# Performance work log

Measured on AMD Instinct MI355X. Metric: run time of the kernel, lower is better.

Reference implementation:

```python
import jax, jax.numpy as jnp
import numpy as np

D_K = 128


def setup_inputs() -> dict:
    key = jax.random.key(0)
    kq, kk, kv = jax.random.split(key, 3)
    S = 8192
    Query = jax.random.normal(kq, (S, D_K), dtype=jnp.float32)
    Key = jax.random.normal(kk, (S, D_K), dtype=jnp.float32)
    Value = jax.random.normal(kv, (S, D_K), dtype=jnp.float32)
    return {"Query": Query, "Key": Key, "Value": Value}


def reference(Query, Key, Value):
    # scaled dot-product attention, unmasked (masked=False default)
    scale = 1.0 / jnp.sqrt(jnp.asarray(D_K, dtype=jnp.float32))
    scores = jnp.matmul(Query, Key.T) * scale          # [S, S]
    attn = jax.nn.softmax(scores, axis=1)              # softmax over keys (dim=1 on 2-D)
    delta_E = jnp.matmul(attn, Value)                  # [S, d_k]
    return delta_E
```

## Files before the change

kernel.cpp:

```cpp
#include <hip/hip_runtime.h>

#define S_LEN 8192
#define D_KK  128
#define SCALE 0.08838834764831845f

typedef __bf16 bf16x2 __attribute__((ext_vector_type(2)));
typedef __bf16 bf16x4 __attribute__((ext_vector_type(4)));
typedef __bf16 bf16x8 __attribute__((ext_vector_type(8)));
typedef float  f32x16 __attribute__((ext_vector_type(16)));
typedef _Float16 half_t;

__global__ __launch_bounds__(256) void prep_kv_23450521436217(
    const float* __restrict__ K,
    const float* __restrict__ V,
    __bf16* __restrict__ Kf,
    __bf16* __restrict__ Vf)
{
    const int tid = threadIdx.x;
    const int t   = blockIdx.x;
    __shared__ __bf16 T[32][140];

    const float* ktile = K + (size_t)t * 32 * D_KK;
    const float* vtile = V + (size_t)t * 32 * D_KK;

    const int row = tid & 31;
    const int cp  = tid >> 5;
    #pragma unroll
    for (int i = 0; i < 2; ++i) {
        int c = cp * 2 + i;
        int s = c >> 1, hi = c & 1;
        const float* src = ktile + row * D_KK + c * 8;
        float4 a = *(const float4*)(src);
        float4 b = *(const float4*)(src + 4);
        bf16x8 o;
        o[0]=(__bf16)a.x; o[1]=(__bf16)a.y; o[2]=(__bf16)a.z; o[3]=(__bf16)a.w;
        o[4]=(__bf16)b.x; o[5]=(__bf16)b.y; o[6]=(__bf16)b.z; o[7]=(__bf16)b.w;
        *(bf16x8*)(Kf + (size_t)(t * 8 + s) * 512 + hi * 256 + row * 8) = o;
    }

    #pragma unroll
    for (int i = 0; i < 4; ++i) {
        int f4 = tid + i * 256;
        float4 v = ((const float4*)vtile)[f4];
        int r = f4 >> 5, cc = (f4 & 31) << 2;
        bf16x4 b;
        b[0]=(__bf16)v.x; b[1]=(__bf16)v.y; b[2]=(__bf16)v.z; b[3]=(__bf16)v.w;
        *(bf16x4*)(&T[r][cc]) = b;
    }
    __syncthreads();

    #pragma unroll
    for (int i = 0; i < 2; ++i) {
        int idx  = tid + i * 256;
        int frag = idx >> 6, lane = idx & 63;
        int hi = lane >> 5, l5 = lane & 31;
        int d = frag >> 1, h = frag & 1;
        bf16x8 o;
        #pragma unroll
        for (int j = 0; j < 8; ++j) o[j] = T[16 * h + 8 * hi + j][32 * d + l5];
        *(bf16x8*)(Vf + (size_t)(t * 8 + frag) * 512 + lane * 8) = o;
    }
}

__global__ __launch_bounds__(512, 2) void attn_part_23450521436217(
    const float*  __restrict__ Q,
    const __bf16* __restrict__ Kf,
    const __bf16* __restrict__ Vf,
    half_t* __restrict__ P16,
    float*  __restrict__ Mp,
    float*  __restrict__ Lp)
{
    const int tid  = threadIdx.x;
    const int wave = tid >> 6;
    const int lane = tid & 63;
    const int l5   = lane & 31;
    const int hi   = lane >> 5;

    const int ks   = blockIdx.x & 7;
    const int qt   = blockIdx.x >> 3;
    const int qsub = qt * 8 + wave;
    const int qrow = qsub * 32 + l5;

    __shared__ __align__(16) __bf16 Klds[2][4096];

    bf16x8 qf[8];
    #pragma unroll
    for (int s = 0; s < 8; ++s) {
        const float* qp = Q + (size_t)qrow * D_KK + s * 16 + hi * 8;
        float4 a = *(const float4*)(qp);
        float4 b = *(const float4*)(qp + 4);
        bf16x8 f;
        f[0]=(__bf16)(a.x*SCALE); f[1]=(__bf16)(a.y*SCALE);
        f[2]=(__bf16)(a.z*SCALE); f[3]=(__bf16)(a.w*SCALE);
        f[4]=(__bf16)(b.x*SCALE); f[5]=(__bf16)(b.y*SCALE);
        f[6]=(__bf16)(b.z*SCALE); f[7]=(__bf16)(b.w*SCALE);
        qf[s] = f;
    }

    f32x16 oacc[4];
    #pragma unroll
    for (int d = 0; d < 4; ++d) oacc[d] = f32x16{};
    float m_run = -1e30f, l_run = 0.0f;

    const __bf16* kbase = Kf + (size_t)(ks * 32) * 4096;
    const __bf16* vfp   = Vf + (size_t)(ks * 32) * 4096 + lane * 8;

    {
        const __bf16* src = kbase + wave * 512 + lane * 8;
        __builtin_amdgcn_global_load_lds(
            (const __attribute__((address_space(1))) void*)src,
            (__attribute__((address_space(3))) void*)&Klds[0][wave * 512],
            16, 0, 0);
    }
    __syncthreads();

    for (int it = 0; it < 32; ++it) {
        const int cur = it & 1;

        if (it < 31) {
            const __bf16* src = kbase + (size_t)(it + 1) * 4096 + wave * 512 + lane * 8;
            __builtin_amdgcn_global_load_lds(
                (const __attribute__((address_space(1))) void*)src,
                (__attribute__((address_space(3))) void*)&Klds[cur ^ 1][wave * 512],
                16, 0, 0);
        }

        const __bf16* vt = vfp + (size_t)it * 4096;
        bf16x8 vb[8];
        #pragma unroll
        for (int f = 0; f < 8; ++f) vb[f] = *(const bf16x8*)(vt + f * 512);

        f32x16 c = f32x16{};
        __builtin_amdgcn_s_setprio(1);
        #pragma unroll
        for (int s = 0; s < 8; ++s) {
            bf16x8 kf = *(const bf16x8*)(&Klds[cur][s * 512 + lane * 8]);
            c = __builtin_amdgcn_mfma_f32_32x32x16_bf16(kf, qf[s], c, 0, 0, 0);
        }
        __builtin_amdgcn_s_setprio(0);

        float x0 = fmaxf(c[0], c[8]),  x1 = fmaxf(c[1], c[9]);
        float x2 = fmaxf(c[2], c[10]), x3 = fmaxf(c[3], c[11]);
        float x4 = fmaxf(c[4], c[12]), x5 = fmaxf(c[5], c[13]);
        float x6 = fmaxf(c[6], c[14]), x7 = fmaxf(c[7], c[15]);
        float y0 = fmaxf(fmaxf(x0, x4), fmaxf(x1, x5));
        float y1 = fmaxf(fmaxf(x2, x6), fmaxf(x3, x7));
        float tmax = fmaxf(y0, y1);
        tmax = fmaxf(tmax, __shfl_xor(tmax, 32));
        if (__any(tmax > m_run + 8.0f)) {
            float mnew  = fmaxf(m_run, tmax);
            float alpha = __expf(m_run - mnew);
            #pragma unroll
            for (int d = 0; d < 4; ++d) oacc[d] *= alpha;
            l_run *= alpha;
            m_run  = mnew;
        }
        float p[16];
        #pragma unroll
        for (int r = 0; r < 16; ++r) p[r] = __expf(c[r] - m_run);
        float s0a = (p[0]+p[1]) + (p[2]+p[3]),   s1a = (p[4]+p[5]) + (p[6]+p[7]);
        float s2a = (p[8]+p[9]) + (p[10]+p[11]), s3a = (p[12]+p[13]) + (p[14]+p[15]);
        float ps = (s0a + s1a) + (s2a + s3a);
        ps += __shfl_xor(ps, 32);
        l_run += ps;

        unsigned pk[8];
        #pragma unroll
        for (int tq = 0; tq < 8; ++tq) {
            bf16x2 w; w[0] = (__bf16)p[2*tq]; w[1] = (__bf16)p[2*tq+1];
            pk[tq] = __builtin_bit_cast(unsigned, w);
        }
        asm volatile("v_permlane32_swap_b32 %0, %1" : "+v"(pk[0]), "+v"(pk[2]));
        asm volatile("v_permlane32_swap_b32 %0, %1" : "+v"(pk[1]), "+v"(pk[3]));
        asm volatile("v_permlane32_swap_b32 %0, %1" : "+v"(pk[4]), "+v"(pk[6]));
        asm volatile("v_permlane32_swap_b32 %0, %1" : "+v"(pk[5]), "+v"(pk[7]));
        union { unsigned u[4]; bf16x8 f; } b0, b1;
        b0.u[0]=pk[0]; b0.u[1]=pk[1]; b0.u[2]=pk[2]; b0.u[3]=pk[3];
        b1.u[0]=pk[4]; b1.u[1]=pk[5]; b1.u[2]=pk[6]; b1.u[3]=pk[7];

        __builtin_amdgcn_s_setprio(1);
        #pragma unroll
        for (int d = 0; d < 4; ++d) {
            oacc[d] = __builtin_amdgcn_mfma_f32_32x32x16_bf16(vb[2*d+0], b0.f,
                                                              oacc[d], 0,0,0);
            oacc[d] = __builtin_amdgcn_mfma_f32_32x32x16_bf16(vb[2*d+1], b1.f,
                                                              oacc[d], 0,0,0);
        }
        __builtin_amdgcn_s_setprio(0);

        __syncthreads();
    }

    if (lane < 32) {
        Mp[ks * S_LEN + qrow] = m_run;
        Lp[ks * S_LEN + qrow] = l_run;
    }
    half_t* pb = P16 + (size_t)(ks * 256 + qsub) * (128 * 32);
    #pragma unroll
    for (int d = 0; d < 4; ++d)
        #pragma unroll
        for (int reg = 0; reg < 16; ++reg) {
            int drow = d * 32 + (reg & 3) + 8 * (reg >> 2) + 4 * hi;
            pb[drow * 32 + l5] = (half_t)oacc[d][reg];
        }
}

__global__ __launch_bounds__(256) void attn_merge_23450521436217(
    const half_t* __restrict__ P16,
    const float*  __restrict__ Mp,
    const float*  __restrict__ Lp,
    float* __restrict__ O)
{
    const int tid  = threadIdx.x;
    const int qsub = blockIdx.x;

    __shared__ float W[8][32];
    __shared__ float Li[32];
    __shared__ float Ot[128][33];

    if (tid < 32) {
        const int qrow = qsub * 32 + tid;
        float m[8], l[8];
        #pragma unroll
        for (int ks = 0; ks < 8; ++ks) {
            m[ks] = Mp[ks * S_LEN + qrow];
            l[ks] = Lp[ks * S_LEN + qrow];
        }
        float M = m[0];
        #pragma unroll
        for (int ks = 1; ks < 8; ++ks) M = fmaxf(M, m[ks]);
        float L = 0.0f;
        #pragma unroll
        for (int ks = 0; ks < 8; ++ks) {
            float w = __expf(m[ks] - M);
            W[ks][tid] = w;
            L += l[ks] * w;
        }
        Li[tid] = 1.0f / L;
    }
    __syncthreads();

    const int q  = tid & 31;
    const int dg = tid >> 5;
    #pragma unroll
    for (int j = 0; j < 16; ++j) {
        const int d = dg * 16 + j;
        float acc = 0.0f;
        #pragma unroll
        for (int ks = 0; ks < 8; ++ks)
            acc += W[ks][q] *
                   (float)P16[(size_t)(ks * 256 + qsub) * (128 * 32) + d * 32 + q];
        Ot[d][q] = acc;
    }
    __syncthreads();

    const int qq = tid >> 3;
    const int dv = (tid & 7) * 16;
    const float il = Li[qq];
    float* op = O + (size_t)(qsub * 32 + qq) * D_KK + dv;
    #pragma unroll
    for (int i = 0; i < 4; ++i) {
        float4 o;
        o.x = Ot[dv + i*4 + 0][qq] * il;
        o.y = Ot[dv + i*4 + 1][qq] * il;
        o.z = Ot[dv + i*4 + 2][qq] * il;
        o.w = Ot[dv + i*4 + 3][qq] * il;
        ((float4*)op)[i] = o;
    }
}

extern "C" void kernel_launch(void* const* d_in, const int* in_sizes, int n_in,
                              void* d_out, int out_size, void* d_ws, size_t ws_size,
                              hipStream_t stream) {
    const float* Q = (const float*)d_in[0];
    const float* K = (const float*)d_in[1];
    const float* V = (const float*)d_in[2];
    float* O = (float*)d_out;

    char* ws = (char*)d_ws;
    const size_t kf_b = (size_t)S_LEN * D_KK * 2;
    __bf16* Kf = (__bf16*)(ws);
    __bf16* Vf = (__bf16*)(ws + kf_b);
    float*  Mp = (float*) (ws + 2 * kf_b);
    float*  Lp = (float*) (ws + 2 * kf_b + 8 * S_LEN * 4);
    half_t* P16= (half_t*)(ws + 2 * kf_b + 16 * S_LEN * 4);

    hipLaunchKernelGGL(prep_kv_23450521436217, dim3(S_LEN/32), dim3(256), 0, stream,
                       K, V, Kf, Vf);
    hipLaunchKernelGGL(attn_part_23450521436217, dim3(256), dim3(512), 0, stream,
                       Q, Kf, Vf, P16, Mp, Lp);
    hipLaunchKernelGGL(attn_merge_23450521436217, dim3(S_LEN/32), dim3(256), 0, stream,
                       P16, Mp, Lp, O);
}
```

Measured before the change: 63.83 us.

## Split each block's KV range across two wave groups and fold log2e into Q scale

After: 228.7 us. 258% more time.

```diff
diff --git a/kernel.cpp b/kernel.cpp
--- a/kernel.cpp
+++ b/kernel.cpp
@@ -2,7 +2,7 @@
 
 #define S_LEN 8192
 #define D_KK  128
-#define SCALE 0.08838834764831845f
+#define SCALE2 (0.08838834764831845f * 1.44269504088896340f)
 
 typedef __bf16 bf16x2 __attribute__((ext_vector_type(2)));
 typedef __bf16 bf16x4 __attribute__((ext_vector_type(4)));
@@ -62,7 +62,7 @@
     }
 }
 
-__global__ __launch_bounds__(512, 2) void attn_part_23450521436217(
+__global__ __launch_bounds__(1024, 4) void attn_part_23450521436217(
     const float*  __restrict__ Q,
     const __bf16* __restrict__ Kf,
     const __bf16* __restrict__ Vf,
@@ -75,13 +75,16 @@
     const int lane = tid & 63;
     const int l5   = lane & 31;
     const int hi   = lane >> 5;
+    const int wq   = wave & 7;
+    const int kvh  = wave >> 3;
 
     const int ks   = blockIdx.x & 7;
     const int qt   = blockIdx.x >> 3;
-    const int qsub = qt * 8 + wave;
+    const int qsub = qt * 8 + wq;
     const int qrow = qsub * 32 + l5;
 
-    __shared__ __align__(16) __bf16 Klds[2][4096];
+    __shared__ __align__(16) __bf16 Klds[2][2][4096];
+    __shared__ float Mx[8][32], Lx[8][32];
 
     bf16x8 qf[8];
     #pragma unroll
@@ -90,10 +93,10 @@
         float4 a = *(const float4*)(qp);
         float4 b = *(const float4*)(qp + 4);
         bf16x8 f;
-        f[0]=(__bf16)(a.x*SCALE); f[1]=(__bf16)(a.y*SCALE);
-        f[2]=(__bf16)(a.z*SCALE); f[3]=(__bf16)(a.w*SCALE);
-        f[4]=(__bf16)(b.x*SCALE); f[5]=(__bf16)(b.y*SCALE);
-        f[6]=(__bf16)(b.z*SCALE); f[7]=(__bf16)(b.w*SCALE);
+        f[0]=(__bf16)(a.x*SCALE2); f[1]=(__bf16)(a.y*SCALE2);
+        f[2]=(__bf16)(a.z*SCALE2); f[3]=(__bf16)(a.w*SCALE2);
+        f[4]=(__bf16)(b.x*SCALE2); f[5]=(__bf16)(b.y*SCALE2);
+        f[6]=(__bf16)(b.z*SCALE2); f[7]=(__bf16)(b.w*SCALE2);
         qf[s] = f;
     }
 
@@ -102,26 +105,26 @@
     for (int d = 0; d < 4; ++d) oacc[d] = f32x16{};
     float m_run = -1e30f, l_run = 0.0f;
 
-    const __bf16* kbase = Kf + (size_t)(ks * 32) * 4096;
-    const __bf16* vfp   = Vf + (size_t)(ks * 32) * 4096 + lane * 8;
+    const __bf16* kbase = Kf + (size_t)(ks * 32 + kvh * 16) * 4096;
+    const __bf16* vfp   = Vf + (size_t)(ks * 32 + kvh * 16) * 4096 + lane * 8;
 
     {
-        const __bf16* src = kbase + wave * 512 + lane * 8;
+        const __bf16* src = kbase + wq * 512 + lane * 8;
         __builtin_amdgcn_global_load_lds(
             (const __attribute__((address_space(1))) void*)src,
-            (__attribute__((address_space(3))) void*)&Klds[0][wave * 512],
+            (__attribute__((address_space(3))) void*)&Klds[kvh][0][wq * 512],
             16, 0, 0);
     }
     __syncthreads();
 
-    for (int it = 0; it < 32; ++it) {
+    for (int it = 0; it < 16; ++it) {
         const int cur = it & 1;
 
-        if (it < 31) {
-            const __bf16* src = kbase + (size_t)(it + 1) * 4096 + wave * 512 + lane * 8;
+        if (it < 15) {
+            const __bf16* src = kbase + (size_t)(it + 1) * 4096 + wq * 512 + lane * 8;
             __builtin_amdgcn_global_load_lds(
                 (const __attribute__((address_space(1))) void*)src,
-                (__attribute__((address_space(3))) void*)&Klds[cur ^ 1][wave * 512],
+                (__attribute__((address_space(3))) void*)&Klds[kvh][cur ^ 1][wq * 512],
                 16, 0, 0);
         }
 
@@ -134,7 +137,7 @@
         __builtin_amdgcn_s_setprio(1);
         #pragma unroll
         for (int s = 0; s < 8; ++s) {
-            bf16x8 kf = *(const bf16x8*)(&Klds[cur][s * 512 + lane * 8]);
+            bf16x8 kf = *(const bf16x8*)(&Klds[kvh][cur][s * 512 + lane * 8]);
             c = __builtin_amdgcn_mfma_f32_32x32x16_bf16(kf, qf[s], c, 0, 0, 0);
         }
         __builtin_amdgcn_s_setprio(0);
@@ -147,9 +150,9 @@
         float y1 = fmaxf(fmaxf(x2, x6), fmaxf(x3, x7));
         float tmax = fmaxf(y0, y1);
         tmax = fmaxf(tmax, __shfl_xor(tmax, 32));
-        if (__any(tmax > m_run + 8.0f)) {
+        if (__any(tmax > m_run + 11.5f)) {
             float mnew  = fmaxf(m_run, tmax);
-            float alpha = __expf(m_run - mnew);
+            float alpha = exp2f(m_run - mnew);
             #pragma unroll
             for (int d = 0; d < 4; ++d) oacc[d] *= alpha;
             l_run *= alpha;
@@ -157,7 +160,7 @@
         }
         float p[16];
         #pragma unroll
-        for (int r = 0; r < 16; ++r) p[r] = __expf(c[r] - m_run);
+        for (int r = 0; r < 16; ++r) p[r] = exp2f(c[r] - m_run);
         float s0a = (p[0]+p[1]) + (p[2]+p[3]),   s1a = (p[4]+p[5]) + (p[6]+p[7]);
         float s2a = (p[8]+p[9]) + (p[10]+p[11]), s3a = (p[12]+p[13]) + (p[14]+p[15]);
         float ps = (s0a + s1a) + (s2a + s3a);
@@ -191,18 +194,43 @@
         __syncthreads();
     }
 
-    if (lane < 32) {
-        Mp[ks * S_LEN + qrow] = m_run;
-        Lp[ks * S_LEN + qrow] = l_run;
-    }
-    half_t* pb = P16 + (size_t)(ks * 256 + qsub) * (128 * 32);
-    #pragma unroll
-    for (int d = 0; d < 4; ++d)
-        #pragma unroll
-        for (int reg = 0; reg < 16; ++reg) {
-            int drow = d * 32 + (reg & 3) + 8 * (reg >> 2) + 4 * hi;
-            pb[drow * 32 + l5] = (half_t)oacc[d][reg];
-        }
+    half_t* mrgbase = (half_t*)Klds;
+
+    if (kvh == 1 && lane < 32) { Mx[wq][lane] = m_run; Lx[wq][lane] = l_run; }
+
+    for (int r = 0; r < 2; ++r) {
+        if (kvh == 1 && (wq >> 2) == r) {
+            half_t* mb = mrgbase + (size_t)(wq & 3) * 4096;
+            #pragma unroll
+            for (int d = 0; d < 4; ++d)
+                #pragma unroll
+                for (int reg = 0; reg < 16; ++reg) {
+                    int drow = d * 32 + (reg & 3) + 8 * (reg >> 2) + 4 * hi;
+                    mb[drow * 32 + l5] = (half_t)oacc[d][reg];
+                }
+        }
+        __syncthreads();
+        if (kvh == 0 && (wq >> 2) == r) {
+            float m1 = Mx[wq][l5], l1 = Lx[wq][l5];
+            float M  = fmaxf(m_run, m1);
+            float w0 = exp2f(m_run - M), w1 = exp2f(m1 - M);
+            if (lane < 32) {
+                Mp[ks * S_LEN + qrow] = M;
+                Lp[ks * S_LEN + qrow] = l_run * w0 + l1 * w1;
+            }
+            const half_t* mb = mrgbase + (size_t)(wq & 3) * 4096;
+            half_t* pb = P16 + (size_t)(ks * 256 + qsub) * 4096;
+            #pragma unroll
+            for (int d = 0; d < 4; ++d)
+                #pragma unroll
+                for (int reg = 0; reg < 16; ++reg) {
+                    int drow = d * 32 + (reg & 3) + 8 * (reg >> 2) + 4 * hi;
+                    pb[drow * 32 + l5] =
+                        (half_t)(oacc[d][reg] * w0 + (float)mb[drow * 32 + l5] * w1);
+                }
+        }
+        __syncthreads();
+    }
 }
 
 __global__ __launch_bounds__(256) void attn_merge_23450521436217(
@@ -232,7 +260,7 @@
         float L = 0.0f;
         #pragma unroll
         for (int ks = 0; ks < 8; ++ks) {
-            float w = __expf(m[ks] - M);
+            float w = exp2f(m[ks] - M);
             W[ks][tid] = w;
             L += l[ks] * w;
         }
@@ -287,7 +315,7 @@
 
     hipLaunchKernelGGL(prep_kv_23450521436217, dim3(S_LEN/32), dim3(256), 0, stream,
                        K, V, Kf, Vf);
-    hipLaunchKernelGGL(attn_part_23450521436217, dim3(256), dim3(512), 0, stream,
+    hipLaunchKernelGGL(attn_part_23450521436217, dim3(256), dim3(1024), 0, stream,
                        Q, Kf, Vf, P16, Mp, Lp);
     hipLaunchKernelGGL(attn_merge_23450521436217, dim3(S_LEN/32), dim3(256), 0, stream,
                        P16, Mp, Lp, O);
```

## Split output head dimension across two wave groups and use exp2 softmax

Applied to the files above, without the earlier changes.

Result: slower. 90.56 us (+41.9%).

```diff
diff --git a/kernel.cpp b/kernel.cpp
--- a/kernel.cpp
+++ b/kernel.cpp
@@ -2,7 +2,7 @@
 
 #define S_LEN 8192
 #define D_KK  128
-#define SCALE 0.08838834764831845f
+#define SCALE2 (0.08838834764831845f * 1.44269504088896340f)
 
 typedef __bf16 bf16x2 __attribute__((ext_vector_type(2)));
 typedef __bf16 bf16x4 __attribute__((ext_vector_type(4)));
@@ -62,7 +62,7 @@
     }
 }
 
-__global__ __launch_bounds__(512, 2) void attn_part_23450521436217(
+__global__ __launch_bounds__(1024, 1) void attn_part_23450521436217(
     const float*  __restrict__ Q,
     const __bf16* __restrict__ Kf,
     const __bf16* __restrict__ Vf,
@@ -75,10 +75,12 @@
     const int lane = tid & 63;
     const int l5   = lane & 31;
     const int hi   = lane >> 5;
+    const int wq   = wave & 7;
+    const int dh   = wave >> 3;
 
     const int ks   = blockIdx.x & 7;
     const int qt   = blockIdx.x >> 3;
-    const int qsub = qt * 8 + wave;
+    const int qsub = qt * 8 + wq;
     const int qrow = qsub * 32 + l5;
 
     __shared__ __align__(16) __bf16 Klds[2][4096];
@@ -90,26 +92,25 @@
         float4 a = *(const float4*)(qp);
         float4 b = *(const float4*)(qp + 4);
         bf16x8 f;
-        f[0]=(__bf16)(a.x*SCALE); f[1]=(__bf16)(a.y*SCALE);
-        f[2]=(__bf16)(a.z*SCALE); f[3]=(__bf16)(a.w*SCALE);
-        f[4]=(__bf16)(b.x*SCALE); f[5]=(__bf16)(b.y*SCALE);
-        f[6]=(__bf16)(b.z*SCALE); f[7]=(__bf16)(b.w*SCALE);
+        f[0]=(__bf16)(a.x*SCALE2); f[1]=(__bf16)(a.y*SCALE2);
+        f[2]=(__bf16)(a.z*SCALE2); f[3]=(__bf16)(a.w*SCALE2);
+        f[4]=(__bf16)(b.x*SCALE2); f[5]=(__bf16)(b.y*SCALE2);
+        f[6]=(__bf16)(b.z*SCALE2); f[7]=(__bf16)(b.w*SCALE2);
         qf[s] = f;
     }
 
-    f32x16 oacc[4];
-    #pragma unroll
-    for (int d = 0; d < 4; ++d) oacc[d] = f32x16{};
+    f32x16 oacc0 = f32x16{}, oacc1 = f32x16{};
     float m_run = -1e30f, l_run = 0.0f;
 
     const __bf16* kbase = Kf + (size_t)(ks * 32) * 4096;
-    const __bf16* vfp   = Vf + (size_t)(ks * 32) * 4096 + lane * 8;
-
-    {
-        const __bf16* src = kbase + wave * 512 + lane * 8;
+    const __bf16* vfp   = Vf + (size_t)(ks * 32) * 4096 + lane * 8
+                             + (size_t)(dh * 4) * 512;
+
+    if (dh == 0) {
+        const __bf16* src = kbase + wq * 512 + lane * 8;
         __builtin_amdgcn_global_load_lds(
             (const __attribute__((address_space(1))) void*)src,
-            (__attribute__((address_space(3))) void*)&Klds[0][wave * 512],
+            (__attribute__((address_space(3))) void*)&Klds[0][wq * 512],
             16, 0, 0);
     }
     __syncthreads();
@@ -117,18 +118,13 @@
     for (int it = 0; it < 32; ++it) {
         const int cur = it & 1;
 
-        if (it < 31) {
-            const __bf16* src = kbase + (size_t)(it + 1) * 4096 + wave * 512 + lane * 8;
+        if (dh == 0 && it < 31) {
+            const __bf16* src = kbase + (size_t)(it + 1) * 4096 + wq * 512 + lane * 8;
             __builtin_amdgcn_global_load_lds(
                 (const __attribute__((address_space(1))) void*)src,
-                (__attribute__((address_space(3))) void*)&Klds[cur ^ 1][wave * 512],
+                (__attribute__((address_space(3))) void*)&Klds[cur ^ 1][wq * 512],
                 16, 0, 0);
         }
-
-        const __bf16* vt = vfp + (size_t)it * 4096;
-        bf16x8 vb[8];
-        #pragma unroll
-        for (int f = 0; f < 8; ++f) vb[f] = *(const bf16x8*)(vt + f * 512);
 
         f32x16 c = f32x16{};
         __builtin_amdgcn_s_setprio(1);
@@ -147,17 +143,17 @@
         float y1 = fmaxf(fmaxf(x2, x6), fmaxf(x3, x7));
         float tmax = fmaxf(y0, y1);
         tmax = fmaxf(tmax, __shfl_xor(tmax, 32));
-        if (__any(tmax > m_run + 8.0f)) {
+        if (__any(tmax > m_run + 11.5f)) {
             float mnew  = fmaxf(m_run, tmax);
-            float alpha = __expf(m_run - mnew);
-            #pragma unroll
-            for (int d = 0; d < 4; ++d) oacc[d] *= alpha;
+            float alpha = exp2f(m_run - mnew);
+            oacc0 *= alpha;
+            oacc1 *= alpha;
             l_run *= alpha;
             m_run  = mnew;
         }
         float p[16];
         #pragma unroll
-        for (int r = 0; r < 16; ++r) p[r] = __expf(c[r] - m_run);
+        for (int r = 0; r < 16; ++r) p[r] = exp2f(c[r] - m_run);
         float s0a = (p[0]+p[1]) + (p[2]+p[3]),   s1a = (p[4]+p[5]) + (p[6]+p[7]);
         float s2a = (p[8]+p[9]) + (p[10]+p[11]), s3a = (p[12]+p[13]) + (p[14]+p[15]);
         float ps = (s0a + s1a) + (s2a + s3a);
@@ -178,31 +174,34 @@
         b0.u[0]=pk[0]; b0.u[1]=pk[1]; b0.u[2]=pk[2]; b0.u[3]=pk[3];
         b1.u[0]=pk[4]; b1.u[1]=pk[5]; b1.u[2]=pk[6]; b1.u[3]=pk[7];
 
+        const __bf16* vt = vfp + (size_t)it * 4096;
+        bf16x8 v0 = *(const bf16x8*)(vt);
+        bf16x8 v1 = *(const bf16x8*)(vt + 512);
+        bf16x8 v2 = *(const bf16x8*)(vt + 1024);
+        bf16x8 v3 = *(const bf16x8*)(vt + 1536);
+
         __builtin_amdgcn_s_setprio(1);
-        #pragma unroll
-        for (int d = 0; d < 4; ++d) {
-            oacc[d] = __builtin_amdgcn_mfma_f32_32x32x16_bf16(vb[2*d+0], b0.f,
-                                                              oacc[d], 0,0,0);
-            oacc[d] = __builtin_amdgcn_mfma_f32_32x32x16_bf16(vb[2*d+1], b1.f,
-                                                              oacc[d], 0,0,0);
-        }
+        oacc0 = __builtin_amdgcn_mfma_f32_32x32x16_bf16(v0, b0.f, oacc0, 0, 0, 0);
+        oacc0 = __builtin_amdgcn_mfma_f32_32x32x16_bf16(v1, b1.f, oacc0, 0, 0, 0);
+        oacc1 = __builtin_amdgcn_mfma_f32_32x32x16_bf16(v2, b0.f, oacc1, 0, 0, 0);
+        oacc1 = __builtin_amdgcn_mfma_f32_32x32x16_bf16(v3, b1.f, oacc1, 0, 0, 0);
         __builtin_amdgcn_s_setprio(0);
 
         __syncthreads();
     }
 
-    if (lane < 32) {
+    if (dh == 0 && lane < 32) {
         Mp[ks * S_LEN + qrow] = m_run;
         Lp[ks * S_LEN + qrow] = l_run;
     }
-    half_t* pb = P16 + (size_t)(ks * 256 + qsub) * (128 * 32);
-    #pragma unroll
-    for (int d = 0; d < 4; ++d)
-        #pragma unroll
-        for (int reg = 0; reg < 16; ++reg) {
-            int drow = d * 32 + (reg & 3) + 8 * (reg >> 2) + 4 * hi;
-            pb[drow * 32 + l5] = (half_t)oacc[d][reg];
-        }
+    half_t* pb = P16 + (size_t)(ks * 256 + qsub) * 4096;
+    #pragma unroll
+    for (int reg = 0; reg < 16; ++reg) {
+        int drow0 = (2*dh + 0) * 32 + (reg & 3) + 8 * (reg >> 2) + 4 * hi;
+        int drow1 = (2*dh + 1) * 32 + (reg & 3) + 8 * (reg >> 2) + 4 * hi;
+        pb[drow0 * 32 + l5] = (half_t)oacc0[reg];
+        pb[drow1 * 32 + l5] = (half_t)oacc1[reg];
+    }
 }
 
 __global__ __launch_bounds__(256) void attn_merge_23450521436217(
@@ -232,7 +231,7 @@
         float L = 0.0f;
         #pragma unroll
         for (int ks = 0; ks < 8; ++ks) {
-            float w = __expf(m[ks] - M);
+            float w = exp2f(m[ks] - M);
             W[ks][tid] = w;
             L += l[ks] * w;
         }
@@ -287,7 +286,7 @@
 
     hipLaunchKernelGGL(prep_kv_23450521436217, dim3(S_LEN/32), dim3(256), 0, stream,
                        K, V, Kf, Vf);
-    hipLaunchKernelGGL(attn_part_23450521436217, dim3(256), dim3(512), 0, stream,
+    hipLaunchKernelGGL(attn_part_23450521436217, dim3(256), dim3(1024), 0, stream,
                        Q, Kf, Vf, P16, Mp, Lp);
     hipLaunchKernelGGL(attn_merge_23450521436217, dim3(S_LEN/32), dim3(256), 0, stream,
                        P16, Mp, Lp, O);
```

## Use 16-way KV split and exp2-based softmax with folded log2e scale

Applied to the files above, without the earlier changes.

Result: slower. 111.9 us (+75.4%).

```diff
diff --git a/kernel.cpp b/kernel.cpp
--- a/kernel.cpp
+++ b/kernel.cpp
@@ -2,7 +2,7 @@
 
 #define S_LEN 8192
 #define D_KK  128
-#define SCALE 0.08838834764831845f
+#define SCALE2 (0.08838834764831845f * 1.44269504088896340f)
 
 typedef __bf16 bf16x2 __attribute__((ext_vector_type(2)));
 typedef __bf16 bf16x4 __attribute__((ext_vector_type(4)));
@@ -62,6 +62,7 @@
     }
 }
 
+template<int NS>
 __global__ __launch_bounds__(512, 2) void attn_part_23450521436217(
     const float*  __restrict__ Q,
     const __bf16* __restrict__ Kf,
@@ -70,14 +71,15 @@
     float*  __restrict__ Mp,
     float*  __restrict__ Lp)
 {
+    constexpr int ITERS = 256 / NS;
     const int tid  = threadIdx.x;
     const int wave = tid >> 6;
     const int lane = tid & 63;
     const int l5   = lane & 31;
     const int hi   = lane >> 5;
 
-    const int ks   = blockIdx.x & 7;
-    const int qt   = blockIdx.x >> 3;
+    const int ks   = blockIdx.x & (NS - 1);
+    const int qt   = blockIdx.x / NS;
     const int qsub = qt * 8 + wave;
     const int qrow = qsub * 32 + l5;
 
@@ -90,10 +92,10 @@
         float4 a = *(const float4*)(qp);
         float4 b = *(const float4*)(qp + 4);
         bf16x8 f;
-        f[0]=(__bf16)(a.x*SCALE); f[1]=(__bf16)(a.y*SCALE);
-        f[2]=(__bf16)(a.z*SCALE); f[3]=(__bf16)(a.w*SCALE);
-        f[4]=(__bf16)(b.x*SCALE); f[5]=(__bf16)(b.y*SCALE);
-        f[6]=(__bf16)(b.z*SCALE); f[7]=(__bf16)(b.w*SCALE);
+        f[0]=(__bf16)(a.x*SCALE2); f[1]=(__bf16)(a.y*SCALE2);
+        f[2]=(__bf16)(a.z*SCALE2); f[3]=(__bf16)(a.w*SCALE2);
+        f[4]=(__bf16)(b.x*SCALE2); f[5]=(__bf16)(b.y*SCALE2);
+        f[6]=(__bf16)(b.z*SCALE2); f[7]=(__bf16)(b.w*SCALE2);
         qf[s] = f;
     }
 
@@ -102,8 +104,8 @@
     for (int d = 0; d < 4; ++d) oacc[d] = f32x16{};
     float m_run = -1e30f, l_run = 0.0f;
 
-    const __bf16* kbase = Kf + (size_t)(ks * 32) * 4096;
-    const __bf16* vfp   = Vf + (size_t)(ks * 32) * 4096 + lane * 8;
+    const __bf16* kbase = Kf + (size_t)(ks * ITERS) * 4096;
+    const __bf16* vfp   = Vf + (size_t)(ks * ITERS) * 4096 + lane * 8;
 
     {
         const __bf16* src = kbase + wave * 512 + lane * 8;
@@ -114,10 +116,10 @@
     }
     __syncthreads();
 
-    for (int it = 0; it < 32; ++it) {
+    for (int it = 0; it < ITERS; ++it) {
         const int cur = it & 1;
 
-        if (it < 31) {
+        if (it < ITERS - 1) {
             const __bf16* src = kbase + (size_t)(it + 1) * 4096 + wave * 512 + lane * 8;
             __builtin_amdgcn_global_load_lds(
                 (const __attribute__((address_space(1))) void*)src,
@@ -147,9 +149,9 @@
         float y1 = fmaxf(fmaxf(x2, x6), fmaxf(x3, x7));
         float tmax = fmaxf(y0, y1);
         tmax = fmaxf(tmax, __shfl_xor(tmax, 32));
-        if (__any(tmax > m_run + 8.0f)) {
+        if (__any(tmax > m_run + 11.5f)) {
             float mnew  = fmaxf(m_run, tmax);
-            float alpha = __expf(m_run - mnew);
+            float alpha = exp2f(m_run - mnew);
             #pragma unroll
             for (int d = 0; d < 4; ++d) oacc[d] *= alpha;
             l_run *= alpha;
@@ -157,7 +159,7 @@
         }
         float p[16];
         #pragma unroll
-        for (int r = 0; r < 16; ++r) p[r] = __expf(c[r] - m_run);
+        for (int r = 0; r < 16; ++r) p[r] = exp2f(c[r] - m_run);
         float s0a = (p[0]+p[1]) + (p[2]+p[3]),   s1a = (p[4]+p[5]) + (p[6]+p[7]);
         float s2a = (p[8]+p[9]) + (p[10]+p[11]), s3a = (p[12]+p[13]) + (p[14]+p[15]);
         float ps = (s0a + s1a) + (s2a + s3a);
@@ -205,6 +207,7 @@
         }
 }
 
+template<int NS>
 __global__ __launch_bounds__(256) void attn_merge_23450521436217(
     const half_t* __restrict__ P16,
     const float*  __restrict__ Mp,
@@ -214,25 +217,25 @@
     const int tid  = threadIdx.x;
     const int qsub = blockIdx.x;
 
-    __shared__ float W[8][32];
+    __shared__ float W[NS][32];
     __shared__ float Li[32];
     __shared__ float Ot[128][33];
 
     if (tid < 32) {
         const int qrow = qsub * 32 + tid;
-        float m[8], l[8];
-        #pragma unroll
-        for (int ks = 0; ks < 8; ++ks) {
+        float m[NS], l[NS];
+        #pragma unroll
+        for (int ks = 0; ks < NS; ++ks) {
             m[ks] = Mp[ks * S_LEN + qrow];
             l[ks] = Lp[ks * S_LEN + qrow];
         }
         float M = m[0];
         #pragma unroll
-        for (int ks = 1; ks < 8; ++ks) M = fmaxf(M, m[ks]);
+        for (int ks = 1; ks < NS; ++ks) M = fmaxf(M, m[ks]);
         float L = 0.0f;
         #pragma unroll
-        for (int ks = 0; ks < 8; ++ks) {
-            float w = __expf(m[ks] - M);
+        for (int ks = 0; ks < NS; ++ks) {
+            float w = exp2f(m[ks] - M);
             W[ks][tid] = w;
             L += l[ks] * w;
         }
@@ -247,7 +250,7 @@
         const int d = dg * 16 + j;
         float acc = 0.0f;
         #pragma unroll
-        for (int ks = 0; ks < 8; ++ks)
+        for (int ks = 0; ks < NS; ++ks)
             acc += W[ks][q] *
                    (float)P16[(size_t)(ks * 256 + qsub) * (128 * 32) + d * 32 + q];
         Ot[d][q] = acc;
@@ -281,14 +284,27 @@
     const size_t kf_b = (size_t)S_LEN * D_KK * 2;
     __bf16* Kf = (__bf16*)(ws);
     __bf16* Vf = (__bf16*)(ws + kf_b);
-    float*  Mp = (float*) (ws + 2 * kf_b);
-    float*  Lp = (float*) (ws + 2 * kf_b + 8 * S_LEN * 4);
-    half_t* P16= (half_t*)(ws + 2 * kf_b + 16 * S_LEN * 4);
 
     hipLaunchKernelGGL(prep_kv_23450521436217, dim3(S_LEN/32), dim3(256), 0, stream,
                        K, V, Kf, Vf);
-    hipLaunchKernelGGL(attn_part_23450521436217, dim3(256), dim3(512), 0, stream,
-                       Q, Kf, Vf, P16, Mp, Lp);
-    hipLaunchKernelGGL(attn_merge_23450521436217, dim3(S_LEN/32), dim3(256), 0, stream,
-                       P16, Mp, Lp, O);
+
+    const size_t need16 = 2 * kf_b + (size_t)2 * 16 * S_LEN * 4
+                        + (size_t)16 * 256 * 4096 * 2;
+    if (ws_size >= need16) {
+        float*  Mp = (float*) (ws + 2 * kf_b);
+        float*  Lp = (float*) (ws + 2 * kf_b + 16 * S_LEN * 4);
+        half_t* P16= (half_t*)(ws + 2 * kf_b + 32 * S_LEN * 4);
+        hipLaunchKernelGGL((attn_part_23450521436217<16>), dim3(512), dim3(512),
+                           0, stream, Q, Kf, Vf, P16, Mp, Lp);
+        hipLaunchKernelGGL((attn_merge_23450521436217<16>), dim3(S_LEN/32), dim3(256),
+                           0, stream, P16, Mp, Lp, O);
+    } else {
+        float*  Mp = (float*) (ws + 2 * kf_b);
+        float*  Lp = (float*) (ws + 2 * kf_b + 8 * S_LEN * 4);
+        half_t* P16= (half_t*)(ws + 2 * kf_b + 16 * S_LEN * 4);
+        hipLaunchKernelGGL((attn_part_23450521436217<8>), dim3(256), dim3(512),
+                           0, stream, Q, Kf, Vf, P16, Mp, Lp);
+        hipLaunchKernelGGL((attn_merge_23450521436217<8>), dim3(S_LEN/32), dim3(256),
+                           0, stream, P16, Mp, Lp, O);
+    }
 }
```
